# Kernel tuning notes

Measured on AMD Instinct MI355X. Metric: run time of the kernel, lower is better.

The kernel has to match this reference:

```python
import jax, jax.numpy as jnp
import numpy as np

B = 16384    # batch of game states
HAND = 8     # max_hand_size
A = 30       # max_actions
C = 4        # max cards per action combo
E = 32       # card_embed_dim
HID = 128    # hidden_dim


def _encode_cards(cards, val_emb, suit_emb, type_emb):
    # cards: int array, 0 = padding, 53 = joker (treated as padding for value/suit)
    invalid = (cards == 0) | (cards == 53)
    values = jnp.where(invalid, 0, (cards - 1) % 13 + 1)
    suits = jnp.where(invalid, 0, (cards - 1) // 13 + 1)
    ce = jnp.concatenate([val_emb[values], suit_emb[suits]], axis=-1)  # [..., E]
    ct = jnp.where(values == 11, 1, jnp.where(values == 12, 2, jnp.where(values == 13, 3, 0)))
    te = type_emb[ct]  # [..., 8]
    pad = jnp.zeros(te.shape[:-1] + (E - te.shape[-1],), ce.dtype)
    return ce + jnp.concatenate([te, pad], axis=-1)


def _mha(q, kv, wq, bq, wk, bk, wv, bv, wo, bo, nh, kpm=None):
    b, sq, e = q.shape
    sk = kv.shape[1]
    hd = e // nh
    Q = (q @ wq + bq).reshape(b, sq, nh, hd)
    K = (kv @ wk + bk).reshape(b, sk, nh, hd)
    V = (kv @ wv + bv).reshape(b, sk, nh, hd)
    s = jnp.einsum('bqhd,bkhd->bhqk', Q, K) * (1.0 / np.sqrt(hd))
    if kpm is not None:  # kpm True = valid key
        s = s + jnp.where(kpm[:, None, None, :], 0.0, -1e9)
    a = jax.nn.softmax(s, axis=-1)
    o = jnp.einsum('bhqk,bkhd->bqhd', a, V).reshape(b, sq, e)
    return o @ wo + bo


def _combo_features(cards):
    # cards: [A, C] int, 0 = padding. Vectorized version of _compute_combo_features.
    mask = cards != 0
    combo_size = mask.sum(1).astype(jnp.float32)
    values = jnp.where(mask, (cards - 1) % 13 + 1, 0)
    has_valid = mask.any(1)
    fidx = jnp.argmax(mask, axis=1)
    fv = values[jnp.arange(cards.shape[0]), fidx]  # first valid value per action
    same = jnp.where(mask, values == fv[:, None], True).all(1).astype(jnp.float32)
    vf = values.astype(jnp.float32)
    attack = jnp.where(values == 1, 1.0,
             jnp.where(values == 11, 10.0,
             jnp.where(values == 12, 15.0,
             jnp.where(values == 13, 20.0, vf))))
    total = (attack * mask).sum(1)
    suits = jnp.where(mask, (cards - 1) // 13 + 1, 0)
    uniq = jnp.stack([(suits == s).any(1) for s in (1, 2, 3, 4)], 0).sum(0).astype(jnp.float32)
    ace = ((values == 1) & mask).any(1).astype(jnp.float32)
    valid = ((combo_size <= 4.0) & ((same > 0) | (ace > 0))).astype(jnp.float32)
    feats = jnp.stack([combo_size, same, total, uniq, ace, valid], axis=1)  # [A, 6]
    return jnp.where(has_valid[:, None], feats, 0.0), has_valid


def _forward(hand_cards, enemy_card, hand_size, game_state, discard_pile_cards,
             action_card_indices, num_valid_actions,
             val_emb, suit_emb, type_emb,
             ce_w1, ce_b1, ce_w2, ce_b2,
             ha_wq, ha_bq, ha_wk, ha_bk, ha_wv, ha_bv, ha_wo, ha_bo,
             he_wq, he_bq, he_wk, he_bk, he_wv, he_bv, he_wo, he_bo,
             se_w1, se_b1, se_w2, se_b2,
             atc_w1, atc_b1, atc_w2, atc_b2,
             as_w1, as_b1, as_w2, as_b2, as_w3, as_b3,
             cx_w1, cx_b1, cx_w2, cx_b2, cx_w3, cx_b3):
    relu = jax.nn.relu
    hand_emb = _encode_cards(hand_cards, val_emb, suit_emb, type_emb)            # [B, HAND, E]
    enemy_emb = _encode_cards(enemy_card[:, None], val_emb, suit_emb, type_emb)  # [B, 1, E]
    hand_mask = hand_cards != 0
    attended = _mha(hand_emb, hand_emb, ha_wq, ha_bq, ha_wk, ha_bk, ha_wv, ha_bv, ha_wo, ha_bo, 8, kpm=hand_mask)
    ctx_he = _mha(attended, enemy_emb, he_wq, he_bq, he_wk, he_bk, he_wv, he_bv, he_wo, he_bo, 4)
    lengths = jnp.maximum(hand_size.astype(jnp.float32), 1.0)[:, None]
    hand_ctx = ctx_he.sum(1) / lengths                                           # [B, E]

    # strategic features (batched per game state)
    hvals = jnp.where(hand_cards == 0, 0, (hand_cards - 1) % 13 + 1)
    hsz = hand_size.astype(jnp.float32)
    aces = (hvals == 1).sum(1).astype(jnp.float32)
    faces = ((hvals >= 11) & (hvals <= 13)).sum(1).astype(jnp.float32)
    low = ((hvals >= 2) & (hvals <= 6)).sum(1).astype(jnp.float32)
    hsuits = jnp.where(hand_cards == 0, 0, (hand_cards - 1) // 13 + 1)
    scnt = [(hsuits == s).sum(1).astype(jnp.float32) for s in (1, 2, 3, 4)]
    hvr = faces / (hsz + 1e-8)
    sdiv = jnp.stack([(hsuits == s).any(1) for s in (1, 2, 3, 4)], 0).sum(0).astype(jnp.float32) / 4.0
    strat = jnp.stack([hsz, aces, faces, low, scnt[0], scnt[1], scnt[2], scnt[3], hvr, sdiv], axis=1)
    strat_in = jnp.concatenate([game_state, strat], axis=1)                      # [B, 20]
    strat_ctx = relu(strat_in @ se_w1 + se_b1) @ se_w2 + se_b2                   # [B, 32]

    combined = jnp.concatenate([hand_ctx, enemy_emb[:, 0], strat_ctx, discard_pile_cards], axis=1)  # [B, 150]
    h = relu(combined @ cx_w1 + cx_b1)
    h = relu(h @ cx_w2 + cx_b2)
    ctx = h @ cx_w3 + cx_b3                                                      # [B, HID]
    type_probs = jax.nn.softmax(relu(ctx @ atc_w1 + atc_b1) @ atc_w2 + atc_b2, axis=-1)  # [B, 4]

    feats, has_valid = _combo_features(action_card_indices)                      # [A, 6], [A]
    emb = _encode_cards(action_card_indices, val_emb, suit_emb, type_emb)        # [A, C, E]
    m = (action_card_indices != 0).astype(emb.dtype)[..., None]
    cnt = jnp.maximum(m.sum(1), 1.0)
    act_emb = (emb * m).sum(1) / cnt                                             # masked mean over real cards
    act_emb = jnp.where(has_valid[:, None], act_emb, 0.0)
    combo_enc = relu(feats @ ce_w1 + ce_b1) @ ce_w2 + ce_b2                      # [A, 16]

    Bn = ctx.shape[0]
    af = jnp.concatenate([
        jnp.broadcast_to(ctx[:, None, :], (Bn, A, HID)),
        jnp.broadcast_to(act_emb[None], (Bn, A, E)),
        jnp.broadcast_to(combo_enc[None], (Bn, A, 16)),
    ], axis=-1)                                                                  # [B, A, 176]
    s = relu(af @ as_w1 + as_b1)
    s = relu(s @ as_w2 + as_b2)
    score = (s @ as_w3 + as_b3)[..., 0]                                          # [B, A]

    strength = feats[:, 2] / 20.0                                                # [A]
    bonus_valid = type_probs[:, 0:1] * strength[None, :] + type_probs[:, 1:2] * (1.0 - strength[None, :])
    bonus_empty = jnp.broadcast_to(type_probs[:, 3:4] * 2.0, (Bn, A))
    bonus = jnp.where(has_valid[None, :], bonus_valid, bonus_empty)
    return score + bonus                                                          # [B, A]


def setup_inputs() -> dict:
    key = jax.random.key(0)
    ki = iter(jax.random.split(key, 64))
    def nrm(shape, s):
        return (s * jax.random.normal(next(ki), shape)).astype(jnp.float32)
    def lin(i, o, s=0.08):
        return nrm((i, o), s), nrm((o,), 0.02)
    d = {}
    hc = jax.random.randint(next(ki), (B, HAND), 0, 53)
    d['hand_cards'] = hc.at[:, 0].set(jax.random.randint(next(ki), (B,), 1, 53))  # at least one valid card per hand
    d['enemy_card'] = jax.random.randint(next(ki), (B,), 1, 53)
    d['hand_size'] = jax.random.randint(next(ki), (B,), 1, 9)
    d['game_state'] = nrm((B, 10), 1.0)
    d['discard_pile_cards'] = jax.random.uniform(next(ki), (B, 54), dtype=jnp.float32)
    d['action_card_indices'] = jax.random.randint(next(ki), (A, C), 1, 53)
    d['num_valid_actions'] = A
    d['val_emb'] = nrm((14, 16), 0.1).at[0].set(0.0)   # padding_idx=0
    d['suit_emb'] = nrm((5, 16), 0.1).at[0].set(0.0)   # padding_idx=0
    d['type_emb'] = nrm((4, 8), 0.1)
    d['ce_w1'], d['ce_b1'] = lin(6, 32)
    d['ce_w2'], d['ce_b2'] = lin(32, 16)
    for p in ('ha', 'he'):
        for t in ('q', 'k', 'v', 'o'):
            d[p + '_w' + t], d[p + '_b' + t] = lin(E, E)
    d['se_w1'], d['se_b1'] = lin(20, 64)
    d['se_w2'], d['se_b2'] = lin(64, 32)
    d['atc_w1'], d['atc_b1'] = lin(HID, 64)
    d['atc_w2'], d['atc_b2'] = lin(64, 4)
    d['as_w1'], d['as_b1'] = lin(HID + E + 16, 64)
    d['as_w2'], d['as_b2'] = lin(64, 32)
    d['as_w3'], d['as_b3'] = lin(32, 1)
    d['cx_w1'], d['cx_b1'] = lin(2 * E + 32 + 54, HID)
    d['cx_w2'], d['cx_b2'] = lin(HID, HID)
    d['cx_w3'], d['cx_b3'] = lin(HID, HID)
    return d


def reference(hand_cards, enemy_card, hand_size, game_state, discard_pile_cards,
              action_card_indices, num_valid_actions,
              val_emb, suit_emb, type_emb,
              ce_w1, ce_b1, ce_w2, ce_b2,
              ha_wq, ha_bq, ha_wk, ha_bk, ha_wv, ha_bv, ha_wo, ha_bo,
              he_wq, he_bq, he_wk, he_bk, he_wv, he_bv, he_wo, he_bo,
              se_w1, se_b1, se_w2, se_b2,
              atc_w1, atc_b1, atc_w2, atc_b2,
              as_w1, as_b1, as_w2, as_b2, as_w3, as_b3,
              cx_w1, cx_b1, cx_w2, cx_b2, cx_w3, cx_b3):
    return _forward(hand_cards, enemy_card, hand_size, game_state, discard_pile_cards,
                    action_card_indices, num_valid_actions,
                    val_emb, suit_emb, type_emb,
                    ce_w1, ce_b1, ce_w2, ce_b2,
                    ha_wq, ha_bq, ha_wk, ha_bk, ha_wv, ha_bv, ha_wo, ha_bo,
                    he_wq, he_bq, he_wk, he_bk, he_wv, he_bv, he_wo, he_bo,
                    se_w1, se_b1, se_w2, se_b2,
                    atc_w1, atc_b1, atc_w2, atc_b2,
                    as_w1, as_b1, as_w2, as_b2, as_w3, as_b3,
                    cx_w1, cx_b1, cx_w2, cx_b2, cx_w3, cx_b3)
```

## Files before the change

kernel.cpp:

```cpp
#include <hip/hip_runtime.h>
#include <math.h>


#define QOFF(c, r) ((((c) >> 2) * 256) + ((r) * 4) + ((c) & 3))

__device__ __forceinline__ void encode_card32(int c,
                                              const float* __restrict__ val_emb,
                                              const float* __restrict__ suit_emb,
                                              const float* __restrict__ type_emb,
                                              float* e) {
  bool inv = (c == 0) || (c == 53);
  int v = inv ? 0 : ((c - 1) % 13 + 1);
  int s = inv ? 0 : ((c - 1) / 13 + 1);
  int ct = (v == 11) ? 1 : (v == 12) ? 2 : (v == 13) ? 3 : 0;
#pragma unroll
  for (int i = 0; i < 16; ++i) e[i] = val_emb[v * 16 + i];
#pragma unroll
  for (int i = 0; i < 16; ++i) e[16 + i] = suit_emb[s * 16 + i];
#pragma unroll
  for (int i = 0; i < 8; ++i) e[i] += type_emb[ct * 8 + i];
}

__global__ __launch_bounds__(64) void action_kernel(
    const int* __restrict__ acards,
    const float* __restrict__ val_emb, const float* __restrict__ suit_emb,
    const float* __restrict__ type_emb,
    const float* __restrict__ ce_w1, const float* __restrict__ ce_b1,
    const float* __restrict__ ce_w2, const float* __restrict__ ce_b2,
    const float* __restrict__ as_w1, const float* __restrict__ as_b1,
    float* __restrict__ ws) {
  __shared__ float sAct[30][32];
  __shared__ float sCombo[30][16];
  const int tid = threadIdx.x;

  if (tid < 30) {
    int c[4];
#pragma unroll
    for (int i = 0; i < 4; ++i) c[i] = acards[tid * 4 + i];
    bool mask[4]; int vals[4], suits[4]; int csize = 0; bool hasv = false;
#pragma unroll
    for (int i = 0; i < 4; ++i) {
      mask[i] = (c[i] != 0);
      if (mask[i]) { csize++; hasv = true; }
      vals[i] = mask[i] ? ((c[i] - 1) % 13 + 1) : 0;
      suits[i] = mask[i] ? ((c[i] - 1) / 13 + 1) : 0;
    }
    int fvv = mask[0] ? vals[0] : mask[1] ? vals[1] : mask[2] ? vals[2]
              : mask[3] ? vals[3] : vals[0];
    bool same = true;
#pragma unroll
    for (int i = 0; i < 4; ++i) if (mask[i] && vals[i] != fvv) same = false;
    float total = 0.f;
#pragma unroll
    for (int i = 0; i < 4; ++i) {
      if (mask[i]) {
        int v = vals[i];
        total += (v == 1) ? 1.f : (v == 11) ? 10.f : (v == 12) ? 15.f
                 : (v == 13) ? 20.f : (float)v;
      }
    }
    float uniq = 0.f;
#pragma unroll
    for (int s = 1; s <= 4; ++s) {
      bool any = false;
#pragma unroll
      for (int i = 0; i < 4; ++i) if (suits[i] == s) any = true;
      uniq += any ? 1.f : 0.f;
    }
    bool ace = false;
#pragma unroll
    for (int i = 0; i < 4; ++i) if (mask[i] && vals[i] == 1) ace = true;
    float f_same = same ? 1.f : 0.f, f_ace = ace ? 1.f : 0.f;
    float valid = (((float)csize <= 4.f) && (f_same > 0.f || f_ace > 0.f)) ? 1.f : 0.f;
    float feats[6] = {(float)csize, f_same, total, uniq, f_ace, valid};
    if (!hasv) { for (int i = 0; i < 6; ++i) feats[i] = 0.f; }
    float emb[32];
#pragma unroll
    for (int i = 0; i < 32; ++i) emb[i] = 0.f;
    float cnt = 0.f;
#pragma unroll
    for (int i = 0; i < 4; ++i) {
      float e[32];
      encode_card32(c[i], val_emb, suit_emb, type_emb, e);
      if (mask[i]) {
#pragma unroll
        for (int j = 0; j < 32; ++j) emb[j] += e[j];
        cnt += 1.f;
      }
    }
    float invc = 1.f / fmaxf(cnt, 1.f);
#pragma unroll
    for (int j = 0; j < 32; ++j) sAct[tid][j] = hasv ? emb[j] * invc : 0.f;
    float t32[32];
#pragma unroll
    for (int j = 0; j < 32; ++j) {
      float acc = ce_b1[j];
#pragma unroll
      for (int k = 0; k < 6; ++k) acc += feats[k] * ce_w1[k * 32 + j];
      t32[j] = fmaxf(acc, 0.f);
    }
#pragma unroll
    for (int j = 0; j < 16; ++j) {
      float acc = ce_b2[j];
#pragma unroll
      for (int k = 0; k < 32; ++k) acc += t32[k] * ce_w2[k * 16 + j];
      sCombo[tid][j] = acc;
    }
    ws[1920 + tid] = total * 0.05f;
    ws[1950 + tid] = hasv ? 1.f : 0.f;
  }
  __syncthreads();
  for (int idx = tid; idx < 1920; idx += 64) {
    int a = idx >> 6, j = idx & 63;
    float acc = as_b1[j];
#pragma unroll
    for (int k = 0; k < 32; ++k) acc += sAct[a][k] * as_w1[(128 + k) * 64 + j];
#pragma unroll
    for (int k = 0; k < 16; ++k) acc += sCombo[a][k] * as_w1[(160 + k) * 64 + j];
    ws[idx] = acc;
  }
}

template <int K, int NJ, bool RELU, bool HASB, bool QIN, bool QOUT>
__device__ __forceinline__ void layerU(
    const float* __restrict__ in, int inColBase, float* __restrict__ outB,
    int outColBase, const float* __restrict__ W, int ldw, int j0,
    const float* __restrict__ bias, int r) {
  float acc[NJ];
#pragma unroll
  for (int j = 0; j < NJ; ++j) acc[j] = HASB ? bias[j0 + j] : 0.f;
  if constexpr (QIN) {
    static_assert(K % 4 == 0, "quad input needs K%4==0");
    const int g0 = inColBase >> 2;
#pragma unroll 4
    for (int g = 0; g < K / 4; ++g) {
      float4 a = *(const float4*)&in[(g0 + g) * 256 + r * 4];
#pragma unroll
      for (int q = 0; q < 4; ++q) {
        float av = (q == 0) ? a.x : (q == 1) ? a.y : (q == 2) ? a.z : a.w;
        const float* wr = W + (size_t)(g * 4 + q) * ldw + j0;
#pragma unroll
        for (int j = 0; j < NJ; ++j) acc[j] += av * wr[j];
      }
    }
  } else {
#pragma unroll 4
    for (int k = 0; k < K; ++k) {
      float a = in[(inColBase + k) * 64 + r];
      const float* wr = W + (size_t)k * ldw + j0;
#pragma unroll
      for (int j = 0; j < NJ; ++j) acc[j] += a * wr[j];
    }
  }
#pragma unroll
  for (int j = 0; j < NJ; ++j) if (RELU) acc[j] = fmaxf(acc[j], 0.f);
  if constexpr (QOUT && NJ == 8) {
    const int c0 = outColBase + j0;
    float4 o0 = make_float4(acc[0], acc[1], acc[2], acc[3]);
    float4 o1 = make_float4(acc[4], acc[5], acc[6], acc[7]);
    *(float4*)&outB[(c0 >> 2) * 256 + r * 4] = o0;
    *(float4*)&outB[((c0 >> 2) + 1) * 256 + r * 4] = o1;
  } else if constexpr (QOUT) {
#pragma unroll
    for (int j = 0; j < NJ; ++j) outB[QOFF(outColBase + j0 + j, r)] = acc[j];
  } else {
#pragma unroll
    for (int j = 0; j < NJ; ++j) outB[(outColBase + j0 + j) * 64 + r] = acc[j];
  }
}

__global__ __launch_bounds__(1024) void policy_main(
    const int* __restrict__ hand_cards, const int* __restrict__ enemy_card,
    const int* __restrict__ hand_size, const float* __restrict__ game_state,
    const float* __restrict__ discard,
    const float* __restrict__ val_emb, const float* __restrict__ suit_emb,
    const float* __restrict__ type_emb,
    const float* __restrict__ he_wv, const float* __restrict__ he_bv,
    const float* __restrict__ he_wo, const float* __restrict__ he_bo,
    const float* __restrict__ se_w1, const float* __restrict__ se_b1,
    const float* __restrict__ se_w2, const float* __restrict__ se_b2,
    const float* __restrict__ atc_w1, const float* __restrict__ atc_b1,
    const float* __restrict__ atc_w2, const float* __restrict__ atc_b2,
    const float* __restrict__ as_w1,
    const float* __restrict__ as_w2, const float* __restrict__ as_b2,
    const float* __restrict__ as_w3, const float* __restrict__ as_b3,
    const float* __restrict__ cx_w1, const float* __restrict__ cx_b1,
    const float* __restrict__ cx_w2, const float* __restrict__ cx_b2,
    const float* __restrict__ cx_w3, const float* __restrict__ cx_b3,
    const float* __restrict__ ws, float* __restrict__ out) {
  __shared__ float bufA[128 * 64];
  __shared__ float bufB[128 * 64];

  const int tid = threadIdx.x;
  const int r = tid & 63;
  const int wq = __builtin_amdgcn_readfirstlane(tid >> 6);
  const int b0 = blockIdx.x * 64;

  if (wq == 2) {
#pragma unroll
    for (int k = 0; k < 10; ++k)
      bufB[k * 64 + r] = game_state[(size_t)(b0 + r) * 10 + k];
  }
  if (wq == 0) {
    const int b = b0 + r;
    const float hsz = (float)hand_size[b];
    int aces = 0, faces = 0, low = 0, c1 = 0, c2 = 0, c3 = 0, c4 = 0;
#pragma unroll
    for (int i = 0; i < 8; ++i) {
      int c = hand_cards[b * 8 + i];
      int v = (c == 0) ? 0 : ((c - 1) % 13 + 1);
      int s = (c == 0) ? 0 : ((c - 1) / 13 + 1);
      aces += (v == 1);
      faces += (v >= 11 && v <= 13);
      low += (v >= 2 && v <= 6);
      c1 += (s == 1); c2 += (s == 2); c3 += (s == 3); c4 += (s == 4);
    }
    float sdiv = (float)((c1 > 0) + (c2 > 0) + (c3 > 0) + (c4 > 0)) * 0.25f;
    float hvr = (float)faces / (hsz + 1e-8f);
    bufB[(10 + 0) * 64 + r] = hsz;          bufB[(10 + 1) * 64 + r] = (float)aces;
    bufB[(10 + 2) * 64 + r] = (float)faces; bufB[(10 + 3) * 64 + r] = (float)low;
    bufB[(10 + 4) * 64 + r] = (float)c1;    bufB[(10 + 5) * 64 + r] = (float)c2;
    bufB[(10 + 6) * 64 + r] = (float)c3;    bufB[(10 + 7) * 64 + r] = (float)c4;
    bufB[(10 + 8) * 64 + r] = hvr;          bufB[(10 + 9) * 64 + r] = sdiv;
  }
  if (wq == 1) {
    const int b = b0 + r;
    bufB[116 * 64 + r] = 8.0f / fmaxf((float)hand_size[b], 1.0f);
    float e[32];
    encode_card32(enemy_card[b], val_emb, suit_emb, type_emb, e);
#pragma unroll
    for (int g = 0; g < 8; ++g) {
      float4 ev = make_float4(e[g * 4], e[g * 4 + 1], e[g * 4 + 2], e[g * 4 + 3]);
      *(float4*)&bufA[(8 + g) * 256 + r * 4] = ev;
    }
  }
  __syncthreads();

  layerU<20, 4, true, true, false, false>(bufB, 0, bufB, 20, se_w1, 64, wq * 4,
                                          se_b1, r);
  __syncthreads();

  layerU<64, 2, false, true, false, true>(bufB, 20, bufA, 64, se_w2, 32, wq * 2,
                                          se_b2, r);
  layerU<32, 2, false, true, true, false>(bufA, 32, bufB, 84, he_wv, 32, wq * 2,
                                          he_bv, r);
  __syncthreads();

  {
    const int j0 = wq * 2;
    float acc0 = he_bo[j0], acc1 = he_bo[j0 + 1];
#pragma unroll 4
    for (int k = 0; k < 32; ++k) {
      float a = bufB[(84 + k) * 64 + r];
      const float* wr = he_wo + (size_t)k * 32 + j0;
      acc0 += a * wr[0];
      acc1 += a * wr[1];
    }
    float scale = bufB[116 * 64 + r];
    bufA[QOFF(j0, r)] = scale * acc0;
    bufA[QOFF(j0 + 1, r)] = scale * acc1;
  }
  __syncthreads();

  {
    const int j0 = wq * 8;
    float acc[8];
#pragma unroll
    for (int j = 0; j < 8; ++j) acc[j] = cx_b1[j0 + j];
#pragma unroll 4
    for (int g = 0; g < 24; ++g) {
      float4 a = *(const float4*)&bufA[g * 256 + r * 4];
#pragma unroll
      for (int q = 0; q < 4; ++q) {
        float av = (q == 0) ? a.x : (q == 1) ? a.y : (q == 2) ? a.z : a.w;
        const float* wr = cx_w1 + (size_t)(g * 4 + q) * 128 + j0;
#pragma unroll
        for (int j = 0; j < 8; ++j) acc[j] += av * wr[j];
      }
    }
    const float* drow = discard + (size_t)(b0 + r) * 54;
#pragma unroll 2
    for (int k = 0; k < 54; ++k) {
      float a = drow[k];
      const float* wr = cx_w1 + (size_t)(96 + k) * 128 + j0;
#pragma unroll
      for (int j = 0; j < 8; ++j) acc[j] += a * wr[j];
    }
    float4 o0 = make_float4(fmaxf(acc[0], 0.f), fmaxf(acc[1], 0.f),
                            fmaxf(acc[2], 0.f), fmaxf(acc[3], 0.f));
    float4 o1 = make_float4(fmaxf(acc[4], 0.f), fmaxf(acc[5], 0.f),
                            fmaxf(acc[6], 0.f), fmaxf(acc[7], 0.f));
    *(float4*)&bufB[(j0 >> 2) * 256 + r * 4] = o0;
    *(float4*)&bufB[((j0 >> 2) + 1) * 256 + r * 4] = o1;
  }
  __syncthreads();

  layerU<128, 8, true, true, true, true>(bufB, 0, bufA, 0, cx_w2, 128, wq * 8,
                                         cx_b2, r);
  __syncthreads();

  layerU<128, 8, false, true, true, true>(bufA, 0, bufB, 0, cx_w3, 128, wq * 8,
                                          cx_b3, r);
  __syncthreads();

  if (wq < 8) {
    layerU<128, 8, true, true, true, true>(bufB, 0, bufA, 0, atc_w1, 64, wq * 8,
                                           atc_b1, r);
  } else {
    layerU<128, 8, false, false, true, true>(bufB, 0, bufA, 64, as_w1, 64,
                                             (wq - 8) * 8, nullptr, r);
  }
  __syncthreads();

  if (wq < 4) {
    float acc = atc_b2[wq];
#pragma unroll 4
    for (int g = 0; g < 16; ++g) {
      float4 t = *(const float4*)&bufA[g * 256 + r * 4];
      acc += t.x * atc_w2[(g * 4 + 0) * 4 + wq];
      acc += t.y * atc_w2[(g * 4 + 1) * 4 + wq];
      acc += t.z * atc_w2[(g * 4 + 2) * 4 + wq];
      acc += t.w * atc_w2[(g * 4 + 3) * 4 + wq];
    }
    bufB[wq * 64 + r] = acc;
  }
  __syncthreads();

  if (wq < 15) {
    float l0 = bufB[0 * 64 + r], l1 = bufB[1 * 64 + r];
    float l2 = bufB[2 * 64 + r], l3 = bufB[3 * 64 + r];
    float m = fmaxf(fmaxf(l0, l1), fmaxf(l2, l3));
    float e0 = expf(l0 - m), e1 = expf(l1 - m), e2 = expf(l2 - m), e3 = expf(l3 - m);
    float inv = 1.f / (e0 + e1 + e2 + e3);
    float tp0 = e0 * inv, tp1 = e1 * inv, tp3 = e3 * inv;

    const float b3v = as_b3[0];
#pragma unroll 1
    for (int i = 0; i < 2; ++i) {
      const int a = wq * 2 + i;
      const float* qa = ws + a * 64;
      float acc[32];
#pragma unroll
      for (int j = 0; j < 32; ++j) acc[j] = 0.f;
#pragma unroll 2
      for (int g = 0; g < 16; ++g) {
        float4 pv = *(const float4*)&bufA[(16 + g) * 256 + r * 4];
#pragma unroll
        for (int q = 0; q < 4; ++q) {
          float p = (q == 0) ? pv.x : (q == 1) ? pv.y : (q == 2) ? pv.z : pv.w;
          const int k = g * 4 + q;
          float s = fmaxf(p + qa[k], 0.f);
          const float* w2r = as_w2 + (size_t)k * 32;
#pragma unroll
          for (int j = 0; j < 32; ++j) acc[j] += s * w2r[j];
        }
      }
      float sc = b3v;
#pragma unroll
      for (int j = 0; j < 32; ++j)
        sc += fmaxf(acc[j] + as_b2[j], 0.f) * as_w3[j];
      float st = ws[1920 + a], hv = ws[1950 + a];
      float bon = (hv > 0.5f) ? (tp0 * st + tp1 * (1.f - st)) : tp3 * 2.f;
      out[(size_t)(b0 + r) * 30 + a] = sc + bon;
    }
  }
}

extern "C" void kernel_launch(void* const* d_in, const int* in_sizes, int n_in,
                              void* d_out, int out_size, void* d_ws, size_t ws_size,
                              hipStream_t stream) {
  (void)in_sizes; (void)n_in; (void)out_size; (void)ws_size;
  const int* hand_cards = (const int*)d_in[0];
  const int* enemy_card = (const int*)d_in[1];
  const int* hand_size = (const int*)d_in[2];
  const float* game_state = (const float*)d_in[3];
  const float* discard = (const float*)d_in[4];
  const int* acards = (const int*)d_in[5];
  const float* val_emb = (const float*)d_in[7];
  const float* suit_emb = (const float*)d_in[8];
  const float* type_emb = (const float*)d_in[9];
  const float* ce_w1 = (const float*)d_in[10], * ce_b1 = (const float*)d_in[11];
  const float* ce_w2 = (const float*)d_in[12], * ce_b2 = (const float*)d_in[13];
  const float* he_wv = (const float*)d_in[26], * he_bv = (const float*)d_in[27];
  const float* he_wo = (const float*)d_in[28], * he_bo = (const float*)d_in[29];
  const float* se_w1 = (const float*)d_in[30], * se_b1 = (const float*)d_in[31];
  const float* se_w2 = (const float*)d_in[32], * se_b2 = (const float*)d_in[33];
  const float* atc_w1 = (const float*)d_in[34], * atc_b1 = (const float*)d_in[35];
  const float* atc_w2 = (const float*)d_in[36], * atc_b2 = (const float*)d_in[37];
  const float* as_w1 = (const float*)d_in[38], * as_b1 = (const float*)d_in[39];
  const float* as_w2 = (const float*)d_in[40], * as_b2 = (const float*)d_in[41];
  const float* as_w3 = (const float*)d_in[42], * as_b3 = (const float*)d_in[43];
  const float* cx_w1 = (const float*)d_in[44], * cx_b1 = (const float*)d_in[45];
  const float* cx_w2 = (const float*)d_in[46], * cx_b2 = (const float*)d_in[47];
  const float* cx_w3 = (const float*)d_in[48], * cx_b3 = (const float*)d_in[49];
  float* ws = (float*)d_ws;
  float* out = (float*)d_out;

  hipLaunchKernelGGL(action_kernel, dim3(1), dim3(64), 0, stream,
                     acards, val_emb, suit_emb, type_emb,
                     ce_w1, ce_b1, ce_w2, ce_b2, as_w1, as_b1, ws);
  hipLaunchKernelGGL(policy_main, dim3(256), dim3(1024), 0, stream,
                     hand_cards, enemy_card, hand_size, game_state, discard,
                     val_emb, suit_emb, type_emb,
                     he_wv, he_bv, he_wo, he_bo,
                     se_w1, se_b1, se_w2, se_b2,
                     atc_w1, atc_b1, atc_w2, atc_b2,
                     as_w1, as_w2, as_b2, as_w3, as_b3,
                     cx_w1, cx_b1, cx_w2, cx_b2, cx_w3, cx_b3,
                     ws, out);
}
```

Before: 244.1 us.

## Stage discard rows in LDS and rebalance early state-encoder layers across waves

The 54-wide discard rows are now loaded cooperatively and coalesced into the quad-interleaved shared buffer at kernel start, so the cx_w1 layer reads them from LDS instead of issuing strided per-thread global loads. The buffer grows to hold them. The small state-encoder and hand-enemy value and output layers are repartitioned so that two independent chains run on separate wave groups with wider per-wave output slices, which removes one barrier. Quad stores are generalised to float4 writes for any multiple of four. The cost is more LDS per block and the extra 54-column pass over shared memory.

```diff
diff --git a/kernel.cpp b/kernel.cpp
--- a/kernel.cpp
+++ b/kernel.cpp
@@ -1,8 +1,6 @@
 #include <hip/hip_runtime.h>
 #include <math.h>
 
-
-#define QOFF(c, r) ((((c) >> 2) * 256) + ((r) * 4) + ((c) & 3))
 
 __device__ __forceinline__ void encode_card32(int c,
                                               const float* __restrict__ val_emb,
@@ -154,15 +152,14 @@
   }
 #pragma unroll
   for (int j = 0; j < NJ; ++j) if (RELU) acc[j] = fmaxf(acc[j], 0.f);
-  if constexpr (QOUT && NJ == 8) {
+  if constexpr (QOUT && (NJ % 4 == 0)) {
     const int c0 = outColBase + j0;
-    float4 o0 = make_float4(acc[0], acc[1], acc[2], acc[3]);
-    float4 o1 = make_float4(acc[4], acc[5], acc[6], acc[7]);
-    *(float4*)&outB[(c0 >> 2) * 256 + r * 4] = o0;
-    *(float4*)&outB[((c0 >> 2) + 1) * 256 + r * 4] = o1;
-  } else if constexpr (QOUT) {
-#pragma unroll
-    for (int j = 0; j < NJ; ++j) outB[QOFF(outColBase + j0 + j, r)] = acc[j];
+#pragma unroll
+    for (int qg = 0; qg < NJ / 4; ++qg) {
+      float4 o = make_float4(acc[qg * 4], acc[qg * 4 + 1],
+                             acc[qg * 4 + 2], acc[qg * 4 + 3]);
+      *(float4*)&outB[((c0 >> 2) + qg) * 256 + r * 4] = o;
+    }
   } else {
 #pragma unroll
     for (int j = 0; j < NJ; ++j) outB[(outColBase + j0 + j) * 64 + r] = acc[j];
@@ -188,7 +185,7 @@
     const float* __restrict__ cx_w2, const float* __restrict__ cx_b2,
     const float* __restrict__ cx_w3, const float* __restrict__ cx_b3,
     const float* __restrict__ ws, float* __restrict__ out) {
-  __shared__ float bufA[128 * 64];
+  __shared__ float bufA[38 * 256];
   __shared__ float bufB[128 * 64];
 
   const int tid = threadIdx.x;
@@ -196,6 +193,11 @@
   const int wq = __builtin_amdgcn_readfirstlane(tid >> 6);
   const int b0 = blockIdx.x * 64;
 
+  for (int idx = tid; idx < 64 * 54; idx += 1024) {
+    int rr = idx / 54, k = idx - rr * 54;
+    int c = 96 + k;
+    bufA[(c >> 2) * 256 + rr * 4 + (c & 3)] = discard[(size_t)b0 * 54 + idx];
+  }
   if (wq == 2) {
 #pragma unroll
     for (int k = 0; k < 10; ++k)
@@ -236,29 +238,34 @@
   }
   __syncthreads();
 
-  layerU<20, 4, true, true, false, false>(bufB, 0, bufB, 20, se_w1, 64, wq * 4,
-                                          se_b1, r);
-  __syncthreads();
-
-  layerU<64, 2, false, true, false, true>(bufB, 20, bufA, 64, se_w2, 32, wq * 2,
-                                          se_b2, r);
-  layerU<32, 2, false, true, true, false>(bufA, 32, bufB, 84, he_wv, 32, wq * 2,
-                                          he_bv, r);
-  __syncthreads();
-
-  {
-    const int j0 = wq * 2;
-    float acc0 = he_bo[j0], acc1 = he_bo[j0 + 1];
+  if (wq < 8) {
+    layerU<20, 8, true, true, false, false>(bufB, 0, bufB, 20, se_w1, 64,
+                                            wq * 8, se_b1, r);
+  } else {
+    layerU<32, 4, false, true, true, false>(bufA, 32, bufB, 84, he_wv, 32,
+                                            (wq - 8) * 4, he_bv, r);
+  }
+  __syncthreads();
+
+  if (wq < 8) {
+    layerU<64, 4, false, true, false, true>(bufB, 20, bufA, 64, se_w2, 32,
+                                            wq * 4, se_b2, r);
+  } else {
+    const int j0 = (wq - 8) * 4;
+    float acc[4];
+#pragma unroll
+    for (int j = 0; j < 4; ++j) acc[j] = he_bo[j0 + j];
 #pragma unroll 4
     for (int k = 0; k < 32; ++k) {
       float a = bufB[(84 + k) * 64 + r];
       const float* wr = he_wo + (size_t)k * 32 + j0;
-      acc0 += a * wr[0];
-      acc1 += a * wr[1];
+#pragma unroll
+      for (int j = 0; j < 4; ++j) acc[j] += a * wr[j];
     }
     float scale = bufB[116 * 64 + r];
-    bufA[QOFF(j0, r)] = scale * acc0;
-    bufA[QOFF(j0 + 1, r)] = scale * acc1;
+    float4 o = make_float4(scale * acc[0], scale * acc[1],
+                           scale * acc[2], scale * acc[3]);
+    *(float4*)&bufA[(j0 >> 2) * 256 + r * 4] = o;
   }
   __syncthreads();
 
@@ -268,7 +275,7 @@
 #pragma unroll
     for (int j = 0; j < 8; ++j) acc[j] = cx_b1[j0 + j];
 #pragma unroll 4
-    for (int g = 0; g < 24; ++g) {
+    for (int g = 0; g < 37; ++g) {
       float4 a = *(const float4*)&bufA[g * 256 + r * 4];
 #pragma unroll
       for (int q = 0; q < 4; ++q) {
@@ -278,20 +285,19 @@
         for (int j = 0; j < 8; ++j) acc[j] += av * wr[j];
       }
     }
-    const float* drow = discard + (size_t)(b0 + r) * 54;
-#pragma unroll 2
-    for (int k = 0; k < 54; ++k) {
-      float a = drow[k];
-      const float* wr = cx_w1 + (size_t)(96 + k) * 128 + j0;
-#pragma unroll
-      for (int j = 0; j < 8; ++j) acc[j] += a * wr[j];
-    }
-    float4 o0 = make_float4(fmaxf(acc[0], 0.f), fmaxf(acc[1], 0.f),
-                            fmaxf(acc[2], 0.f), fmaxf(acc[3], 0.f));
-    float4 o1 = make_float4(fmaxf(acc[4], 0.f), fmaxf(acc[5], 0.f),
-                            fmaxf(acc[6], 0.f), fmaxf(acc[7], 0.f));
-    *(float4*)&bufB[(j0 >> 2) * 256 + r * 4] = o0;
-    *(float4*)&bufB[((j0 >> 2) + 1) * 256 + r * 4] = o1;
+    {
+      float4 a = *(const float4*)&bufA[37 * 256 + r * 4];
+      const float* wr0 = cx_w1 + (size_t)148 * 128 + j0;
+      const float* wr1 = cx_w1 + (size_t)149 * 128 + j0;
+#pragma unroll
+      for (int j = 0; j < 8; ++j) acc[j] += a.x * wr0[j] + a.y * wr1[j];
+    }
+#pragma unroll
+    for (int qg = 0; qg < 2; ++qg) {
+      float4 o = make_float4(fmaxf(acc[qg * 4], 0.f), fmaxf(acc[qg * 4 + 1], 0.f),
+                             fmaxf(acc[qg * 4 + 2], 0.f), fmaxf(acc[qg * 4 + 3], 0.f));
+      *(float4*)&bufB[((j0 >> 2) + qg) * 256 + r * 4] = o;
+    }
   }
   __syncthreads();
 
@@ -304,8 +310,8 @@
   __syncthreads();
 
   if (wq < 8) {
-    layerU<128, 8, true, true, true, true>(bufB, 0, bufA, 0, atc_w1, 64, wq * 8,
-                                           atc_b1, r);
+    layerU<128, 8, true, true, true, true>(bufB, 0, bufA, 0, atc_w1, 64,
+                                           wq * 8, atc_b1, r);
   } else {
     layerU<128, 8, false, false, true, true>(bufB, 0, bufA, 64, as_w1, 64,
                                              (wq - 8) * 8, nullptr, r);
```

Result: no change. 246.0 us (+0.8%).
